# Kernel tuning notes

Measured on AMD Instinct MI355X. Metric: run time of the kernel, lower is better.

The kernel has to match this reference:

```python
import jax, jax.numpy as jnp
import numpy as np

B, L, D, K = 16, 2048, 128, 8192
NUM_RQ_STEPS = 1


def _nearest(residual, codebook):
    # residual: [B,L,D], codebook: [K,D]
    d2 = (
        jnp.sum(residual * residual, axis=-1, keepdims=True)  # [B,L,1]
        - 2.0 * jnp.einsum('bld,kd->blk', residual, codebook)  # [B,L,K]
        + jnp.sum(codebook * codebook, axis=-1)  # [K]
    )
    idx = jnp.argmin(d2, axis=-1)  # [B,L]
    return codebook[idx], idx  # gather: [B,L,D]


def setup_inputs() -> dict:
    key = jax.random.key(0)
    k1, k2 = jax.random.split(key)
    z_e = jax.random.normal(k1, (B, L, D), dtype=jnp.float32)
    codebook = jax.random.normal(k2, (K, D), dtype=jnp.float32)
    return {"z_e": z_e, "codebook": codebook}


def reference(z_e, codebook):
    # apply_codebook(z_e, code_sg=True): codebook is stop-gradiented,
    # residual quantization over NUM_RQ_STEPS, straight-through on output.
    cb = jax.lax.stop_gradient(codebook)
    residual = z_e
    z_q = jnp.zeros_like(z_e)
    idx_list = []
    for _ in range(NUM_RQ_STEPS):
        q, idx = _nearest(residual, cb)
        z_q = z_q + q
        residual = residual - q
        idx_list.append(idx)
    indices = jnp.stack(idx_list, axis=-1)  # [B,L,num_rq_steps]
    # straight-through estimator (code_sg=True): grads flow to z_e, not codebook
    z_q = z_e + jax.lax.stop_gradient(z_q - z_e)
    return z_q, indices
```

## Files before the change

kernel.cpp:

```cpp
#include <hip/hip_runtime.h>


#define M_TOK  32768
#define DIM    128
#define KCODES 8192
#define BM     64
#define NT     (KCODES / 256)
#define MARGIN 0.10f

typedef _Float16 half8v __attribute__((ext_vector_type(8)));
typedef float float4v __attribute__((ext_vector_type(4)));

union H2U { _Float16 h; unsigned short u; };
__device__ __forceinline__ unsigned short f2h_bits(_Float16 h) {
  H2U c; c.h = h; return c.u;
}

__device__ __forceinline__ void gload_lds16(const void* g, void* l) {
  __builtin_amdgcn_global_load_lds(
      (const __attribute__((address_space(1))) unsigned int*)g,
      (__attribute__((address_space(3))) unsigned int*)l, 16, 0, 0);
}

#define CNORM_OFF  (KCODES * 256)
#define QCNT_OFF   (CNORM_OFF + KCODES * 4)
#define QTOK_OFF   (QCNT_OFF + 64)
#define KMIN_OFF   (QTOK_OFF + M_TOK * 4)

__global__ __launch_bounds__(256) void prep_kernel(
    const float* __restrict__ cb, unsigned short* __restrict__ Cs,
    float* __restrict__ cnorm, int* __restrict__ qcnt) {
  if (blockIdx.x == 0 && threadIdx.x == 0) *qcnt = 0;
  const int k = blockIdx.x * 4 + (threadIdx.x >> 6);
  const int lane = threadIdx.x & 63;
  const float2 v = ((const float2*)(cb + (size_t)k * DIM))[lane];
  float s = v.x * v.x + v.y * v.y;
  #pragma unroll
  for (int off = 32; off > 0; off >>= 1) s += __shfl_down(s, off);
  if (lane == 0) cnorm[k] = s;
  ushort2 hi;
  hi.x = f2h_bits((_Float16)v.x);
  hi.y = f2h_bits((_Float16)v.y);
  *(ushort2*)(Cs + (size_t)k * 128 + lane * 2) = hi;
}

__global__ __launch_bounds__(256, 2) void vq_mfma_kernel(
    const float* __restrict__ ze, const unsigned short* __restrict__ Cs,
    const float* __restrict__ cnorm, const float* __restrict__ cb,
    int* __restrict__ qcnt, int* __restrict__ qtok,
    unsigned long long* __restrict__ kmin,
    float* __restrict__ out_zq, float* __restrict__ out_idx) {
  __shared__ char lds[49152];
  char* const As = lds;
  char* const Bs = lds + 16384;

  const int tid = threadIdx.x;
  const int wn = tid >> 6;
  const int lane = tid & 63;
  const int quad = lane >> 4;
  const int l15 = lane & 15;
  const int m0 = blockIdx.x * BM;

  int loffC[4];
  #pragma unroll
  for (int c = 0; c < 4; ++c) {
    const int r = c * 16 + (lane >> 2);
    const int s = lane & 3;
    const int seg = s ^ ((r >> 1) & 3);
    loffC[c] = (wn * 64 + r) * 256 + seg * 16;
  }
  int boff[4];
  #pragma unroll
  for (int j = 0; j < 4; ++j) {
    const int n = j * 16 + l15;
    boff[j] = n * 64 + ((quad ^ ((n >> 1) & 3)) << 4);
  }
  char* const BsW = Bs + wn * 8192;

  {
    const int r = tid >> 2;
    const int qh = tid & 3;
    const float* zrow = ze + (size_t)(m0 + r) * DIM + qh * 32;
    char* arow = As + r * 256;
    const int rx = r & 7;
    #pragma unroll
    for (int i = 0; i < 8; ++i) {
      const float4 v = *(const float4*)(zrow + i * 4);
      ushort4 hh;
      hh.x = f2h_bits((_Float16)v.x);
      hh.y = f2h_bits((_Float16)v.y);
      hh.z = f2h_bits((_Float16)v.z);
      hh.w = f2h_bits((_Float16)v.w);
      const int c = qh * 32 + i * 4;
      *(ushort4*)(arow + ((((c >> 3) ^ rx) << 4) | ((c & 7) << 1))) = hh;
    }
  }
  __syncthreads();

  half8v ahi[4][4];
  #pragma unroll
  for (int ks = 0; ks < 4; ++ks)
    #pragma unroll
    for (int i = 0; i < 4; ++i) {
      const int m = i * 16 + l15;
      const int kslot = ks * 4 + quad;
      ahi[ks][i] = *(const half8v*)(As + m * 256 + ((kslot ^ (m & 7)) << 4));
    }

  float bestv[16], secv[16], idxv[16];
  #pragma unroll
  for (int s = 0; s < 16; ++s) {
    bestv[s] = 3.4e38f; secv[s] = 3.4e38f; idxv[s] = 0.f;
  }

  for (int nt = 0; nt < NT; ++nt) {
    const char* const tile = (const char*)Cs + (size_t)nt * 65536;
    float cnv[4];
    #pragma unroll
    for (int j = 0; j < 4; ++j)
      cnv[j] = cnorm[nt * 256 + wn * 64 + j * 16 + l15];

    float4v acc[4][4];
    #pragma unroll
    for (int i = 0; i < 4; ++i)
      #pragma unroll
      for (int j = 0; j < 4; ++j) acc[i][j] = (float4v)0.0f;

    #pragma unroll
    for (int t = 0; t < 2; ++t) {
      __syncthreads();
      #pragma unroll
      for (int p = 0; p < 2; ++p)
        #pragma unroll
        for (int c = 0; c < 4; ++c)
          gload_lds16(tile + (t * 2 + p) * 64 + loffC[c],
                      BsW + p * 4096 + c * 1024);
      __syncthreads();

      #pragma unroll
      for (int p = 0; p < 2; ++p) {
        const int kk = t * 2 + p;
        half8v bf[4];
        #pragma unroll
        for (int j = 0; j < 4; ++j)
          bf[j] = *(const half8v*)(BsW + p * 4096 + boff[j]);
        #pragma unroll
        for (int i = 0; i < 4; ++i)
          #pragma unroll
          for (int j = 0; j < 4; ++j)
            acc[i][j] = __builtin_amdgcn_mfma_f32_16x16x32_f16(
                ahi[kk][i], bf[j], acc[i][j], 0, 0, 0);
      }
    }

    #pragma unroll
    for (int j = 0; j < 4; ++j) {
      const float nidx = (float)(nt * 256 + wn * 64 + j * 16 + l15);
      const float cn = cnv[j];
      #pragma unroll
      for (int i = 0; i < 4; ++i)
        #pragma unroll
        for (int rg = 0; rg < 4; ++rg) {
          const float sc = fmaf(-2.0f, acc[i][j][rg], cn);
          const int slot = i * 4 + rg;
          const bool bt = sc < bestv[slot];
          secv[slot] = bt ? bestv[slot] : fminf(secv[slot], sc);
          idxv[slot] = bt ? nidx : idxv[slot];
          bestv[slot] = bt ? sc : bestv[slot];
        }
    }
  }

  #pragma unroll
  for (int slot = 0; slot < 16; ++slot) {
    float b = bestv[slot], sec = secv[slot], ix = idxv[slot];
    #pragma unroll
    for (int mk = 1; mk <= 8; mk <<= 1) {
      const float ob = __shfl_xor(b, mk);
      const float os = __shfl_xor(sec, mk);
      const float oi = __shfl_xor(ix, mk);
      const bool take = (ob < b) || (ob == b && oi < ix);
      const float loser = take ? b : ob;
      b = take ? ob : b;
      ix = take ? oi : ix;
      sec = fminf(fminf(sec, os), loser);
    }
    bestv[slot] = b; secv[slot] = sec; idxv[slot] = ix;
  }

  __syncthreads();
  float* const redB = (float*)lds;
  float* const redS = redB + 256;
  float* const redI = redB + 512;
  float* const lidxs = redB + 768;
  if (l15 == 0) {
    #pragma unroll
    for (int slot = 0; slot < 16; ++slot) {
      const int row = (slot >> 2) * 16 + quad * 4 + (slot & 3);
      redB[wn * 64 + row] = bestv[slot];
      redS[wn * 64 + row] = secv[slot];
      redI[wn * 64 + row] = idxv[slot];
    }
  }
  __syncthreads();
  if (tid < 64) {
    float b = redB[tid], sec = redS[tid], ix = redI[tid];
    #pragma unroll
    for (int w = 1; w < 4; ++w) {
      const float ob = redB[w * 64 + tid];
      const float os = redS[w * 64 + tid];
      const float oi = redI[w * 64 + tid];
      const bool take = (ob < b) || (ob == b && oi < ix);
      const float loser = take ? b : ob;
      b = take ? ob : b;
      ix = take ? oi : ix;
      sec = fminf(fminf(sec, os), loser);
    }
    out_idx[m0 + tid] = ix;
    lidxs[tid] = ix;
    if (sec - b < MARGIN) {
      kmin[m0 + tid] = ~0ull;
      const int p = atomicAdd(qcnt, 1);
      qtok[p] = m0 + tid;
    }
  }
  __syncthreads();

  const int tl = tid >> 2, qp = tid & 3;
  const int code = (int)lidxs[tl];
  const float4* src = (const float4*)(cb + (size_t)code * DIM);
  float4* dst = (float4*)(out_zq + (size_t)(m0 + tl) * DIM);
  #pragma unroll
  for (int p = 0; p < 8; ++p) dst[qp + p * 4] = src[qp + p * 4];
}

__global__ __launch_bounds__(256) void rescan_part_kernel(
    const float* __restrict__ ze, const float* __restrict__ cb,
    const float* __restrict__ cnorm, const int* __restrict__ qcnt,
    const int* __restrict__ qtok, unsigned long long* __restrict__ kmin) {
  __shared__ float xsh[DIM];
  __shared__ float rs[256];
  __shared__ int ri[256];
  const int tid = threadIdx.x;
  const int chunk = blockIdx.x & 31;
  const int n = *qcnt;
  for (int qi = blockIdx.x >> 5; qi < n; qi += (gridDim.x >> 5)) {
    const int token = qtok[qi];
    __syncthreads();
    if (tid < 32)
      ((float4*)xsh)[tid] = ((const float4*)(ze + (size_t)token * DIM))[tid];
    __syncthreads();
    const int code = chunk * 256 + tid;
    const float* crow = cb + (size_t)code * DIM;
    float dot = 0.f;
    #pragma unroll
    for (int d = 0; d < DIM; ++d) dot = fmaf(xsh[d], crow[d], dot);
    rs[tid] = fmaf(-2.f, dot, cnorm[code]);
    ri[tid] = code;
    __syncthreads();
    #pragma unroll
    for (int off = 128; off > 0; off >>= 1) {
      if (tid < off) {
        const float so = rs[tid + off];
        const int io = ri[tid + off];
        if (so < rs[tid] || (so == rs[tid] && io < ri[tid])) {
          rs[tid] = so; ri[tid] = io;
        }
      }
      __syncthreads();
    }
    if (tid == 0) {
      union { float f; unsigned int u; } c; c.f = rs[0];
      const unsigned int m = (c.u >> 31) ? ~c.u : (c.u | 0x80000000u);
      const unsigned long long key =
          ((unsigned long long)m << 32) | (unsigned int)ri[0];
      atomicMin(&kmin[token], key);
    }
    __syncthreads();
  }
}

__global__ __launch_bounds__(256) void rescan_apply_kernel(
    const float* __restrict__ cb, const int* __restrict__ qcnt,
    const int* __restrict__ qtok, const unsigned long long* __restrict__ kmin,
    float* __restrict__ out_zq, float* __restrict__ out_idx) {
  const int tid = threadIdx.x;
  const int n = *qcnt;
  for (int qi = blockIdx.x; qi < n; qi += gridDim.x) {
    const int token = qtok[qi];
    const int code = (int)(unsigned int)(kmin[token] & 0xFFFFFFFFull);
    if (tid == 0) out_idx[token] = (float)code;
    if (tid < 32)
      ((float4*)(out_zq + (size_t)token * DIM))[tid] =
          ((const float4*)(cb + (size_t)code * DIM))[tid];
  }
}

extern "C" void kernel_launch(void* const* d_in, const int* in_sizes, int n_in,
                              void* d_out, int out_size, void* d_ws,
                              size_t ws_size, hipStream_t stream) {
  const float* ze = (const float*)d_in[0];
  const float* cb = (const float*)d_in[1];
  float* out = (float*)d_out;

  unsigned short* Cs = (unsigned short*)d_ws;
  float* cnorm = (float*)((char*)d_ws + CNORM_OFF);
  int* qcnt = (int*)((char*)d_ws + QCNT_OFF);
  int* qtok = (int*)((char*)d_ws + QTOK_OFF);
  unsigned long long* kmin = (unsigned long long*)((char*)d_ws + KMIN_OFF);

  prep_kernel<<<KCODES / 4, 256, 0, stream>>>(cb, Cs, cnorm, qcnt);
  vq_mfma_kernel<<<M_TOK / BM, 256, 0, stream>>>(
      ze, Cs, cnorm, cb, qcnt, qtok, kmin, out, out + (size_t)M_TOK * DIM);
  rescan_part_kernel<<<4096, 256, 0, stream>>>(ze, cb, cnorm, qcnt, qtok,
                                               kmin);
  rescan_apply_kernel<<<256, 256, 0, stream>>>(cb, qcnt, qtok, kmin, out,
                                               out + (size_t)M_TOK * DIM);
}
```

Baseline: 267.0 us.

## Pipeline codebook tile loads per wave with vmcnt waits and fold norm into accumulator

Replaces the block-wide __syncthreads double-phase codebook staging with a per-wave software pipeline. Each wave prefetches the next k-slice (including across tile boundaries) into a ping-pong LDS buffer and waits with explicit s_waitcnt vmcnt/lgkmcnt instead of barriers. The accumulators are initialised to -0.5*||c||^2, so the dot product directly yields a score to maximise. Best and second-best tracking now uses fmax and fmed3, and the next tile's codebook norms are prefetched. Relying on hand-placed waitcnt for correctness of per-wave LDS regions is fragile, and it removes barriers that previously separated the loads.

```diff
diff --git a/kernel.cpp b/kernel.cpp
--- a/kernel.cpp
+++ b/kernel.cpp
@@ -21,6 +21,10 @@
       (const __attribute__((address_space(1))) unsigned int*)g,
       (__attribute__((address_space(3))) unsigned int*)l, 16, 0, 0);
 }
+
+#define WAIT_VMCNT4 asm volatile("s_waitcnt vmcnt(4)" ::: "memory")
+#define WAIT_VMCNT0 asm volatile("s_waitcnt vmcnt(0)" ::: "memory")
+#define WAIT_LGKM0  asm volatile("s_waitcnt lgkmcnt(0)" ::: "memory")
 
 #define CNORM_OFF  (KCODES * 256)
 #define QCNT_OFF   (CNORM_OFF + KCODES * 4)
@@ -77,6 +81,10 @@
   }
   char* const BsW = Bs + wn * 8192;
 
+  float cnv[4];
+  #pragma unroll
+  for (int j = 0; j < 4; ++j) cnv[j] = cnorm[wn * 64 + j * 16 + l15];
+
   {
     const int r = tid >> 2;
     const int qh = tid & 3;
@@ -97,6 +105,13 @@
   }
   __syncthreads();
 
+  #pragma unroll
+  for (int p = 0; p < 2; ++p)
+    #pragma unroll
+    for (int c = 0; c < 4; ++c)
+      gload_lds16((const char*)Cs + p * 64 + loffC[c],
+                  BsW + p * 4096 + c * 1024);
+
   half8v ahi[4][4];
   #pragma unroll
   for (int ks = 0; ks < 4; ++ks)
@@ -110,64 +125,72 @@
   float bestv[16], secv[16], idxv[16];
   #pragma unroll
   for (int s = 0; s < 16; ++s) {
-    bestv[s] = 3.4e38f; secv[s] = 3.4e38f; idxv[s] = 0.f;
+    bestv[s] = -3.4e38f; secv[s] = -3.4e38f; idxv[s] = 0.f;
   }
 
   for (int nt = 0; nt < NT; ++nt) {
-    const char* const tile = (const char*)Cs + (size_t)nt * 65536;
-    float cnv[4];
-    #pragma unroll
-    for (int j = 0; j < 4; ++j)
-      cnv[j] = cnorm[nt * 256 + wn * 64 + j * 16 + l15];
-
     float4v acc[4][4];
     #pragma unroll
-    for (int i = 0; i < 4; ++i)
-      #pragma unroll
-      for (int j = 0; j < 4; ++j) acc[i][j] = (float4v)0.0f;
-
-    #pragma unroll
-    for (int t = 0; t < 2; ++t) {
-      __syncthreads();
-      #pragma unroll
-      for (int p = 0; p < 2; ++p)
+    for (int j = 0; j < 4; ++j) {
+      const float b = -0.5f * cnv[j];
+      #pragma unroll
+      for (int i = 0; i < 4; ++i) {
+        acc[i][j][0] = b; acc[i][j][1] = b;
+        acc[i][j][2] = b; acc[i][j][3] = b;
+      }
+    }
+    float cnvn[4];
+    if (nt + 1 < NT) {
+      #pragma unroll
+      for (int j = 0; j < 4; ++j)
+        cnvn[j] = cnorm[(nt + 1) * 256 + wn * 64 + j * 16 + l15];
+    }
+
+    #pragma unroll
+    for (int kk = 0; kk < 4; ++kk) {
+      const bool more = (kk < 3) || (nt + 1 < NT);
+      if (more && (kk > 0 || nt > 0)) {
+        WAIT_LGKM0;
+        const int ntn = (kk == 3) ? nt + 1 : nt;
+        const int kkn = (kk + 1) & 3;
+        const char* src = (const char*)Cs + (size_t)ntn * 65536 + kkn * 64;
+        char* dst = BsW + ((kk + 1) & 1) * 4096;
         #pragma unroll
         for (int c = 0; c < 4; ++c)
-          gload_lds16(tile + (t * 2 + p) * 64 + loffC[c],
-                      BsW + p * 4096 + c * 1024);
-      __syncthreads();
-
-      #pragma unroll
-      for (int p = 0; p < 2; ++p) {
-        const int kk = t * 2 + p;
-        half8v bf[4];
+          gload_lds16(src + loffC[c], dst + c * 1024);
+      }
+      if (more) { WAIT_VMCNT4; } else { WAIT_VMCNT0; }
+
+      half8v bf[4];
+      #pragma unroll
+      for (int j = 0; j < 4; ++j)
+        bf[j] = *(const half8v*)(BsW + (kk & 1) * 4096 + boff[j]);
+      #pragma unroll
+      for (int i = 0; i < 4; ++i)
         #pragma unroll
         for (int j = 0; j < 4; ++j)
-          bf[j] = *(const half8v*)(BsW + p * 4096 + boff[j]);
-        #pragma unroll
-        for (int i = 0; i < 4; ++i)
-          #pragma unroll
-          for (int j = 0; j < 4; ++j)
-            acc[i][j] = __builtin_amdgcn_mfma_f32_16x16x32_f16(
-                ahi[kk][i], bf[j], acc[i][j], 0, 0, 0);
-      }
+          acc[i][j] = __builtin_amdgcn_mfma_f32_16x16x32_f16(
+              ahi[kk][i], bf[j], acc[i][j], 0, 0, 0);
     }
 
     #pragma unroll
     for (int j = 0; j < 4; ++j) {
       const float nidx = (float)(nt * 256 + wn * 64 + j * 16 + l15);
-      const float cn = cnv[j];
       #pragma unroll
       for (int i = 0; i < 4; ++i)
         #pragma unroll
         for (int rg = 0; rg < 4; ++rg) {
-          const float sc = fmaf(-2.0f, acc[i][j][rg], cn);
+          const float sc = acc[i][j][rg];
           const int slot = i * 4 + rg;
-          const bool bt = sc < bestv[slot];
-          secv[slot] = bt ? bestv[slot] : fminf(secv[slot], sc);
+          const bool bt = sc > bestv[slot];
+          secv[slot] = __builtin_amdgcn_fmed3f(sc, bestv[slot], secv[slot]);
           idxv[slot] = bt ? nidx : idxv[slot];
-          bestv[slot] = bt ? sc : bestv[slot];
+          bestv[slot] = fmaxf(bestv[slot], sc);
         }
+    }
+    if (nt + 1 < NT) {
+      #pragma unroll
+      for (int j = 0; j < 4; ++j) cnv[j] = cnvn[j];
     }
   }
 
@@ -179,11 +202,11 @@
       const float ob = __shfl_xor(b, mk);
       const float os = __shfl_xor(sec, mk);
       const float oi = __shfl_xor(ix, mk);
-      const bool take = (ob < b) || (ob == b && oi < ix);
+      const bool take = (ob > b) || (ob == b && oi < ix);
       const float loser = take ? b : ob;
       b = take ? ob : b;
       ix = take ? oi : ix;
-      sec = fminf(fminf(sec, os), loser);
+      sec = fmaxf(fmaxf(sec, os), loser);
     }
     bestv[slot] = b; secv[slot] = sec; idxv[slot] = ix;
   }
@@ -210,15 +233,15 @@
       const float ob = redB[w * 64 + tid];
       const float os = redS[w * 64 + tid];
       const float oi = redI[w * 64 + tid];
-      const bool take = (ob < b) || (ob == b && oi < ix);
+      const bool take = (ob > b) || (ob == b && oi < ix);
       const float loser = take ? b : ob;
       b = take ? ob : b;
       ix = take ? oi : ix;
-      sec = fminf(fminf(sec, os), loser);
+      sec = fmaxf(fmaxf(sec, os), loser);
     }
     out_idx[m0 + tid] = ix;
     lidxs[tid] = ix;
-    if (sec - b < MARGIN) {
+    if (b - sec < 0.5f * MARGIN) {
       kmin[m0 + tid] = ~0ull;
       const int p = atomicAdd(qcnt, 1);
       qtok[p] = m0 + tid;
```

After: 313.9 us. 17.5% more time.

## Batch rescan over groups of tokens with register tiling and wave-shuffle argmin

Applied to the files above, without the earlier changes.

The fp32 rescan kernel for ambiguous tokens now processes eight queued tokens per block, and each thread covers four codes across a 1024-code chunk instead of one code in a 256-code chunk. Each codebook row load is then reused across eight tokens. The shared-memory tree reduction with many barriers is replaced by wave-level shuffle argmin plus a small cross-wave merge. This cuts codebook reloads and sync overhead in the fallback path, at the cost of more registers (32 accumulators) and possibly lower occupancy. Its weight depends on how many tokens fall within the margin.

```diff
diff --git a/kernel.cpp b/kernel.cpp
--- a/kernel.cpp
+++ b/kernel.cpp
@@ -7,6 +7,7 @@
 #define BM     64
 #define NT     (KCODES / 256)
 #define MARGIN 0.10f
+#define RTG    8
 
 typedef _Float16 half8v __attribute__((ext_vector_type(8)));
 typedef float float4v __attribute__((ext_vector_type(4)));
@@ -238,45 +239,84 @@
     const float* __restrict__ ze, const float* __restrict__ cb,
     const float* __restrict__ cnorm, const int* __restrict__ qcnt,
     const int* __restrict__ qtok, unsigned long long* __restrict__ kmin) {
-  __shared__ float xsh[DIM];
-  __shared__ float rs[256];
-  __shared__ int ri[256];
+  __shared__ float xsh[RTG][132];
+  __shared__ unsigned long long wpart[4][RTG];
   const int tid = threadIdx.x;
-  const int chunk = blockIdx.x & 31;
+  const int wv = tid >> 6;
+  const int lane = tid & 63;
+  const int cg = blockIdx.x & 7;
   const int n = *qcnt;
-  for (int qi = blockIdx.x >> 5; qi < n; qi += (gridDim.x >> 5)) {
-    const int token = qtok[qi];
+  const int nslots = gridDim.x >> 3;
+  const int c0 = cg * 1024 + tid;
+
+  for (int g = blockIdx.x >> 3; g * RTG < n; g += nslots) {
+    const int cnt = min(RTG, n - g * RTG);
     __syncthreads();
-    if (tid < 32)
-      ((float4*)xsh)[tid] = ((const float4*)(ze + (size_t)token * DIM))[tid];
+    if ((tid >> 5) < cnt) {
+      const int token = qtok[g * RTG + (tid >> 5)];
+      const float4 v =
+          ((const float4*)(ze + (size_t)token * DIM))[tid & 31];
+      ((float4*)(xsh[tid >> 5]))[tid & 31] = v;
+    }
     __syncthreads();
-    const int code = chunk * 256 + tid;
-    const float* crow = cb + (size_t)code * DIM;
-    float dot = 0.f;
-    #pragma unroll
-    for (int d = 0; d < DIM; ++d) dot = fmaf(xsh[d], crow[d], dot);
-    rs[tid] = fmaf(-2.f, dot, cnorm[code]);
-    ri[tid] = code;
+
+    float dot[4][RTG];
+    #pragma unroll
+    for (int k = 0; k < 4; ++k)
+      #pragma unroll
+      for (int t = 0; t < RTG; ++t) dot[k][t] = 0.f;
+
+    const float* crow0 = cb + (size_t)c0 * DIM;
+    for (int d = 0; d < DIM; d += 4) {
+      float4 x4[RTG];
+      #pragma unroll
+      for (int t = 0; t < RTG; ++t)
+        x4[t] = *(const float4*)(xsh[t] + d);
+      #pragma unroll
+      for (int k = 0; k < 4; ++k) {
+        const float4 c4 = *(const float4*)(crow0 + (size_t)k * 256 * DIM + d);
+        #pragma unroll
+        for (int t = 0; t < RTG; ++t) {
+          dot[k][t] = fmaf(c4.x, x4[t].x, dot[k][t]);
+          dot[k][t] = fmaf(c4.y, x4[t].y, dot[k][t]);
+          dot[k][t] = fmaf(c4.z, x4[t].z, dot[k][t]);
+          dot[k][t] = fmaf(c4.w, x4[t].w, dot[k][t]);
+        }
+      }
+    }
+
+    float cn[4];
+    #pragma unroll
+    for (int k = 0; k < 4; ++k) cn[k] = cnorm[c0 + k * 256];
+
+    #pragma unroll
+    for (int t = 0; t < RTG; ++t) {
+      float s = fmaf(-2.f, dot[0][t], cn[0]);
+      int ix = c0;
+      #pragma unroll
+      for (int k = 1; k < 4; ++k) {
+        const float sk = fmaf(-2.f, dot[k][t], cn[k]);
+        if (sk < s) { s = sk; ix = c0 + k * 256; }
+      }
+      #pragma unroll
+      for (int mk = 1; mk <= 32; mk <<= 1) {
+        const float os = __shfl_xor(s, mk);
+        const int oi = __shfl_xor(ix, mk);
+        if (os < s || (os == s && oi < ix)) { s = os; ix = oi; }
+      }
+      if (lane == 0) {
+        union { float f; unsigned u; } c; c.f = s;
+        const unsigned m = (c.u >> 31) ? ~c.u : (c.u | 0x80000000u);
+        wpart[wv][t] = ((unsigned long long)m << 32) | (unsigned)ix;
+      }
+    }
     __syncthreads();
-    #pragma unroll
-    for (int off = 128; off > 0; off >>= 1) {
-      if (tid < off) {
-        const float so = rs[tid + off];
-        const int io = ri[tid + off];
-        if (so < rs[tid] || (so == rs[tid] && io < ri[tid])) {
-          rs[tid] = so; ri[tid] = io;
-        }
-      }
-      __syncthreads();
-    }
-    if (tid == 0) {
-      union { float f; unsigned int u; } c; c.f = rs[0];
-      const unsigned int m = (c.u >> 31) ? ~c.u : (c.u | 0x80000000u);
-      const unsigned long long key =
-          ((unsigned long long)m << 32) | (unsigned int)ri[0];
-      atomicMin(&kmin[token], key);
-    }
-    __syncthreads();
+    if (tid < cnt) {
+      unsigned long long k = wpart[0][tid];
+      #pragma unroll
+      for (int w = 1; w < 4; ++w) k = min(k, wpart[w][tid]);
+      atomicMin(&kmin[qtok[g * RTG + tid]], k);
+    }
   }
 }
 
```

New measurement: 255.9 us. 1.04x faster.
